# Kernel tuning notes

Measured on AMD Instinct MI355X. Metric: run time of the kernel, lower is better.

## Reference

```python
import jax, jax.numpy as jnp
import numpy as np

EPS = 1e-5
QMAX = 127.0

def activation_quant(x):
    # per-token (last-dim) abs-max int8 fake-quant
    x_max = jnp.clip(jnp.max(jnp.abs(x), axis=-1, keepdims=True), EPS, None)
    scale = QMAX / x_max
    q = jnp.clip(jnp.round(x * scale), -128.0, 127.0)
    return q / scale

def setup_inputs() -> dict:
    key = jax.random.key(0)
    kx, kw = jax.random.split(key)
    x = jax.random.normal(kx, (4, 8192, 2048), dtype=jnp.float32)
    # ternary {-1, 0, 1} weight, stored int8 in torch, cast to float for the GEMM
    W = jax.random.randint(kw, (2048, 2048), -1, 2).astype(jnp.float32)  # [out, in]
    return {"x": x, "W": W}

def reference(x, W):
    # straight-through estimator form: x + sg(quant(x) - x)
    x_quant = x + jax.lax.stop_gradient(activation_quant(x) - x)
    # y = x_quant @ W.T  (F.linear)
    return jnp.einsum('bsd,od->bso', x_quant, W)
```

## Files before the change

### kernel.cpp

```cpp
#include <hip/hip_runtime.h>

typedef int v4i __attribute__((ext_vector_type(4)));

#define KDIM 2048
#define NDIM 2048

#define GLOAD16(g, l) __builtin_amdgcn_global_load_lds(                      \
    (const __attribute__((address_space(1))) void*)(g),                      \
    (__attribute__((address_space(3))) void*)(l), 16, 0, 0)


__device__ __forceinline__ int pack4q(float4 v, float s) {
  int a = __float2int_rn(v.x * s);
  int b = __float2int_rn(v.y * s);
  int c = __float2int_rn(v.z * s);
  int d = __float2int_rn(v.w * s);
  a = max(-128, min(127, a)); b = max(-128, min(127, b));
  c = max(-128, min(127, c)); d = max(-128, min(127, d));
  return (a & 0xff) | ((b & 0xff) << 8) | ((c & 0xff) << 16) | ((d & 0xff) << 24);
}

__global__ __launch_bounds__(256) void quant_rows(const float* __restrict__ x,
                                                  signed char* __restrict__ q,
                                                  float* __restrict__ rscale) {
  const int row = blockIdx.x;
  const float4* xr = (const float4*)(x + (size_t)row * KDIM);
  float4 v0 = xr[threadIdx.x];
  float4 v1 = xr[256 + threadIdx.x];
  float m = fmaxf(fmaxf(fabsf(v0.x), fabsf(v0.y)), fmaxf(fabsf(v0.z), fabsf(v0.w)));
  m = fmaxf(m, fmaxf(fmaxf(fabsf(v1.x), fabsf(v1.y)), fmaxf(fabsf(v1.z), fabsf(v1.w))));
  #pragma unroll
  for (int off = 32; off > 0; off >>= 1) m = fmaxf(m, __shfl_xor(m, off));
  __shared__ float red[4];
  if ((threadIdx.x & 63) == 0) red[threadIdx.x >> 6] = m;
  __syncthreads();
  float xmax = fmaxf(fmaxf(red[0], red[1]), fmaxf(red[2], red[3]));
  xmax = fmaxf(xmax, 1e-5f);
  const float scale = 127.0f / xmax;
  int* qr = (int*)(q + (size_t)row * KDIM);
  qr[threadIdx.x] = pack4q(v0, scale);
  qr[256 + threadIdx.x] = pack4q(v1, scale);
  if (threadIdx.x == 0) rscale[row] = xmax * (1.0f / 127.0f);
}

__global__ __launch_bounds__(256) void quant_w(const float* __restrict__ W,
                                               signed char* __restrict__ Wq) {
  const int i = blockIdx.x * 256 + threadIdx.x;
  float4 v = ((const float4*)W)[i];
  int a = (int)v.x, b = (int)v.y, c = (int)v.z, d = (int)v.w;
  ((int*)Wq)[i] = (a & 0xff) | ((b & 0xff) << 8) | ((c & 0xff) << 16) | ((d & 0xff) << 24);
}


#define VM4 asm volatile("s_waitcnt vmcnt(4)" ::: "memory")
#define VM0 asm volatile("s_waitcnt vmcnt(0)" ::: "memory")
#define VMNONE

#define STAGE_AB(U, T)                                                       \
  GLOAD16(sa + (T) * 64, lds + (U) * 32768 + dstw);                          \
  GLOAD16(sa + (T) * 64 + 128 * KDIM, lds + (U) * 32768 + 8192 + dstw);      \
  GLOAD16(sb + (T) * 64, lds + (U) * 32768 + 16384 + dstw);                  \
  GLOAD16(sb + (T) * 64 + 128 * KDIM, lds + (U) * 32768 + 24576 + dstw);

#define DECLSET(P) v4i P##b0, P##b1, P##b2, P##b3,                           \
                       P##a0, P##a1, P##a2, P##a3, P##a4, P##a5, P##a6, P##a7;

#define READSET(U, P)                                                        \
  P##b0 = *(const v4i*)(lds + (U) * 32768 + bRd);                            \
  P##b1 = *(const v4i*)(lds + (U) * 32768 + bRd + 1024);                     \
  P##b2 = *(const v4i*)(lds + (U) * 32768 + bRd + 2048);                     \
  P##b3 = *(const v4i*)(lds + (U) * 32768 + bRd + 3072);                     \
  P##a0 = *(const v4i*)(lds + (U) * 32768 + aRd);                            \
  P##a1 = *(const v4i*)(lds + (U) * 32768 + aRd + 1024);                     \
  P##a2 = *(const v4i*)(lds + (U) * 32768 + aRd + 2048);                     \
  P##a3 = *(const v4i*)(lds + (U) * 32768 + aRd + 3072);                     \
  P##a4 = *(const v4i*)(lds + (U) * 32768 + aRd + 4096);                     \
  P##a5 = *(const v4i*)(lds + (U) * 32768 + aRd + 5120);                     \
  P##a6 = *(const v4i*)(lds + (U) * 32768 + aRd + 6144);                     \
  P##a7 = *(const v4i*)(lds + (U) * 32768 + aRd + 7168);

#define MF1(m, n, A, BF) acc[m][n] = __builtin_amdgcn_mfma_i32_16x16x64_i8((A), (BF), acc[m][n], 0, 0, 0);
#define MFROW(m, A, P)                                                       \
  MF1(m, 0, A, P##b0) MF1(m, 1, A, P##b1) MF1(m, 2, A, P##b2) MF1(m, 3, A, P##b3)
#define MFSET(P)                                                             \
  __builtin_amdgcn_s_setprio(1);                                             \
  MFROW(0, P##a0, P) MFROW(1, P##a1, P) MFROW(2, P##a2, P)                   \
  MFROW(3, P##a3, P) MFROW(4, P##a4, P) MFROW(5, P##a5, P)                   \
  MFROW(6, P##a6, P) MFROW(7, P##a7, P)                                      \
  __builtin_amdgcn_s_setprio(0);

#define KTILE(U, T, CUR, NXT, DOREAD, DOSTAGE, VMEND)                        \
  {                                                                          \
    if (DOREAD) { READSET((((U) + 1) & 3), NXT) }                            \
    if (DOSTAGE) { STAGE_AB((((U) + 3) & 3), (T) + 3) }                      \
    __builtin_amdgcn_sched_barrier(0);    \
    MFSET(CUR)                                                               \
    __builtin_amdgcn_sched_barrier(0);                                       \
    VMEND;                                                                   \
    __builtin_amdgcn_s_barrier();                                            \
    __builtin_amdgcn_sched_barrier(0);           \
  }

__global__ __launch_bounds__(512, 2) void gemm_i8(const signed char* __restrict__ A,
                                                  const signed char* __restrict__ B,
                                                  const float* __restrict__ rscale,
                                                  float* __restrict__ C) {
  __shared__ __align__(16) signed char lds[131072];
  const int bid = blockIdx.x;
  const int lid = (bid & 7) * 128 + (bid >> 3);
  const int bm = lid >> 3;
  const int bn = lid & 7;
  const int tid = threadIdx.x;
  const int wid = tid >> 6;
  const int lane = tid & 63;
  const int wr = wid >> 2, wc = wid & 3;

  const int srow = wid * 16 + (lane >> 2);
  const int scol = (((lane & 3) ^ ((lane >> 3) & 3)) << 4);
  const signed char* sa = A + (size_t)(bm * 256 + srow) * KDIM + scol;
  const signed char* sb = B + (size_t)(bn * 256 + srow) * KDIM + scol;
  const int dstw = wid << 10;

  const int rslot = (((lane >> 4) ^ ((lane >> 1) & 3)) << 4);
  const int aRd = (wr * 128 + (lane & 15)) * 64 + rslot;
  const int bRd = 16384 + (wc * 64 + (lane & 15)) * 64 + rslot;

  v4i acc[8][4] = {};
  DECLSET(fX) DECLSET(fY)

  STAGE_AB(0, 0)
  STAGE_AB(1, 1)
  STAGE_AB(2, 2)
  VM4;
  __builtin_amdgcn_s_barrier();
  __builtin_amdgcn_sched_barrier(0);
  READSET(0, fX)

  for (int ti = 0; ti < 7; ++ti) {
    const int t = ti * 4;
    KTILE(0, t + 0, fX, fY, 1, 1, VM4)
    KTILE(1, t + 1, fY, fX, 1, 1, VM4)
    KTILE(2, t + 2, fX, fY, 1, 1, VM4)
    KTILE(3, t + 3, fY, fX, 1, 1, VM4)
  }
  KTILE(0, 28, fX, fY, 1, 1, VM4)
  KTILE(1, 29, fY, fX, 1, 0, VM0)
  KTILE(2, 30, fX, fY, 1, 0, VMNONE)
  KTILE(3, 31, fY, fX, 0, 0, VMNONE)

  const int col0 = bn * 256 + wc * 64 + (lane & 15);
  const int rbase = bm * 256 + wr * 128 + ((lane >> 4) << 2);
  #pragma unroll
  for (int m = 0; m < 8; ++m) {
    #pragma unroll
    for (int r = 0; r < 4; ++r) {
      const int row = rbase + m * 16 + r;
      const float s = rscale[row];
      float* crow = C + (size_t)row * NDIM + col0;
      #pragma unroll
      for (int n = 0; n < 4; ++n) crow[n * 16] = (float)acc[m][n][r] * s;
    }
  }
}

extern "C" void kernel_launch(void* const* d_in, const int* in_sizes, int n_in,
                              void* d_out, int out_size, void* d_ws, size_t ws_size,
                              hipStream_t stream) {
  const float* x = (const float*)d_in[0];
  const float* W = (const float*)d_in[1];
  float* out = (float*)d_out;
  const int M = in_sizes[0] / KDIM;

  signed char* q = (signed char*)d_ws;
  signed char* Wq = q + (size_t)M * KDIM;
  float* rscale = (float*)(Wq + (size_t)NDIM * KDIM);

  quant_rows<<<M, 256, 0, stream>>>(x, q, rscale);
  quant_w<<<(NDIM * KDIM / 4) / 256, 256, 0, stream>>>(W, Wq);
  gemm_i8<<<(M / 256) * (NDIM / 256), 512, 0, stream>>>(q, Wq, rscale, out);
}
```

Baseline: 240.4 us.

## Prepack weights into MFMA fragment layout and load B directly to registers

The weight-quant kernel now writes W in a fragment-ordered layout, so each lane's 16-byte B operand is contiguous. The GEMM loads B straight from global memory into registers instead of staging it through LDS. A is staged alone in a 3-deep LDS ring of 16 KB buffers, which shrinks shared memory from 128 KB to 48 KB and removes B's LDS traffic. The cost is that B fragments are fetched from global/L2 by every wave that needs them, with only one tile of register prefetch to hide that latency.

```diff
diff --git a/kernel.cpp b/kernel.cpp
--- a/kernel.cpp
+++ b/kernel.cpp
@@ -43,69 +43,83 @@
   if (threadIdx.x == 0) rscale[row] = xmax * (1.0f / 127.0f);
 }
 
-__global__ __launch_bounds__(256) void quant_w(const float* __restrict__ W,
-                                               signed char* __restrict__ Wq) {
-  const int i = blockIdx.x * 256 + threadIdx.x;
-  float4 v = ((const float4*)W)[i];
-  int a = (int)v.x, b = (int)v.y, c = (int)v.z, d = (int)v.w;
-  ((int*)Wq)[i] = (a & 0xff) | ((b & 0xff) << 8) | ((c & 0xff) << 16) | ((d & 0xff) << 24);
+__global__ __launch_bounds__(256) void quant_w_pack(const float* __restrict__ W,
+                                                    signed char* __restrict__ Bp) {
+  const int gid = blockIdx.x * 256 + threadIdx.x;
+  const int lane = gid & 63;
+  const int f = gid >> 6;
+  const int nf = f & 15;
+  const int bkt = f >> 4;
+  const int kt = bkt & 31;
+  const int bn = bkt >> 5;
+  const int row = bn * 256 + nf * 16 + (lane & 15);
+  const int k0 = kt * 64 + (lane >> 4) * 16;
+  const float* src = W + (size_t)row * KDIM + k0;
+  int out[4];
+  #pragma unroll
+  for (int j = 0; j < 4; ++j) {
+    int b0 = (int)src[j * 4 + 0] & 0xff;
+    int b1 = (int)src[j * 4 + 1] & 0xff;
+    int b2 = (int)src[j * 4 + 2] & 0xff;
+    int b3 = (int)src[j * 4 + 3] & 0xff;
+    out[j] = b0 | (b1 << 8) | (b2 << 16) | (b3 << 24);
+  }
+  v4i o = { out[0], out[1], out[2], out[3] };
+  *(v4i*)(Bp + (size_t)gid * 16) = o;
 }
 
 
-#define VM4 asm volatile("s_waitcnt vmcnt(4)" ::: "memory")
+#define VM2 asm volatile("s_waitcnt vmcnt(2)" ::: "memory")
 #define VM0 asm volatile("s_waitcnt vmcnt(0)" ::: "memory")
 #define VMNONE
 
-#define STAGE_AB(U, T)                                                       \
-  GLOAD16(sa + (T) * 64, lds + (U) * 32768 + dstw);                          \
-  GLOAD16(sa + (T) * 64 + 128 * KDIM, lds + (U) * 32768 + 8192 + dstw);      \
-  GLOAD16(sb + (T) * 64, lds + (U) * 32768 + 16384 + dstw);                  \
-  GLOAD16(sb + (T) * 64 + 128 * KDIM, lds + (U) * 32768 + 24576 + dstw);
+#define STAGE(U, T)                                                          \
+  GLOAD16(sa + (T) * 64,             lds + (U) * 16384 + dstw);              \
+  GLOAD16(sa + (T) * 64 + 16 * KDIM, lds + (U) * 16384 + 1024 + dstw);
 
-#define DECLSET(P) v4i P##b0, P##b1, P##b2, P##b3,                           \
-                       P##a0, P##a1, P##a2, P##a3, P##a4, P##a5, P##a6, P##a7;
-
-#define READSET(U, P)                                                        \
-  P##b0 = *(const v4i*)(lds + (U) * 32768 + bRd);                            \
-  P##b1 = *(const v4i*)(lds + (U) * 32768 + bRd + 1024);                     \
-  P##b2 = *(const v4i*)(lds + (U) * 32768 + bRd + 2048);                     \
-  P##b3 = *(const v4i*)(lds + (U) * 32768 + bRd + 3072);                     \
-  P##a0 = *(const v4i*)(lds + (U) * 32768 + aRd);                            \
-  P##a1 = *(const v4i*)(lds + (U) * 32768 + aRd + 1024);                     \
-  P##a2 = *(const v4i*)(lds + (U) * 32768 + aRd + 2048);                     \
-  P##a3 = *(const v4i*)(lds + (U) * 32768 + aRd + 3072);                     \
-  P##a4 = *(const v4i*)(lds + (U) * 32768 + aRd + 4096);                     \
-  P##a5 = *(const v4i*)(lds + (U) * 32768 + aRd + 5120);                     \
-  P##a6 = *(const v4i*)(lds + (U) * 32768 + aRd + 6144);                     \
-  P##a7 = *(const v4i*)(lds + (U) * 32768 + aRd + 7168);
+#define LOADB(P, T)                                                          \
+  P##0 = *(const v4i*)(bp + (size_t)(T) * 16384);                            \
+  P##1 = *(const v4i*)(bp + (size_t)(T) * 16384 + 1024);                     \
+  P##2 = *(const v4i*)(bp + (size_t)(T) * 16384 + 2048);                     \
+  P##3 = *(const v4i*)(bp + (size_t)(T) * 16384 + 3072);
 
 #define MF1(m, n, A, BF) acc[m][n] = __builtin_amdgcn_mfma_i32_16x16x64_i8((A), (BF), acc[m][n], 0, 0, 0);
-#define MFROW(m, A, P)                                                       \
-  MF1(m, 0, A, P##b0) MF1(m, 1, A, P##b1) MF1(m, 2, A, P##b2) MF1(m, 3, A, P##b3)
-#define MFSET(P)                                                             \
+
+#define MFSET(CB)                                                            \
   __builtin_amdgcn_s_setprio(1);                                             \
-  MFROW(0, P##a0, P) MFROW(1, P##a1, P) MFROW(2, P##a2, P)                   \
-  MFROW(3, P##a3, P) MFROW(4, P##a4, P) MFROW(5, P##a5, P)                   \
-  MFROW(6, P##a6, P) MFROW(7, P##a7, P)                                      \
+  MF1(0, 0, a0, CB##0) MF1(0, 1, a0, CB##1) MF1(0, 2, a0, CB##2) MF1(0, 3, a0, CB##3) \
+  MF1(1, 0, a1, CB##0) MF1(1, 1, a1, CB##1) MF1(1, 2, a1, CB##2) MF1(1, 3, a1, CB##3) \
+  MF1(2, 0, a2, CB##0) MF1(2, 1, a2, CB##1) MF1(2, 2, a2, CB##2) MF1(2, 3, a2, CB##3) \
+  MF1(3, 0, a3, CB##0) MF1(3, 1, a3, CB##1) MF1(3, 2, a3, CB##2) MF1(3, 3, a3, CB##3) \
+  MF1(4, 0, a4, CB##0) MF1(4, 1, a4, CB##1) MF1(4, 2, a4, CB##2) MF1(4, 3, a4, CB##3) \
+  MF1(5, 0, a5, CB##0) MF1(5, 1, a5, CB##1) MF1(5, 2, a5, CB##2) MF1(5, 3, a5, CB##3) \
+  MF1(6, 0, a6, CB##0) MF1(6, 1, a6, CB##1) MF1(6, 2, a6, CB##2) MF1(6, 3, a6, CB##3) \
+  MF1(7, 0, a7, CB##0) MF1(7, 1, a7, CB##1) MF1(7, 2, a7, CB##2) MF1(7, 3, a7, CB##3) \
   __builtin_amdgcn_s_setprio(0);
 
-#define KTILE(U, T, CUR, NXT, DOREAD, DOSTAGE, VMEND)                        \
+#define KTILE(U, T, CB, NB, DOB, DOSTAGE, VMEND)                             \
   {                                                                          \
-    if (DOREAD) { READSET((((U) + 1) & 3), NXT) }                            \
-    if (DOSTAGE) { STAGE_AB((((U) + 3) & 3), (T) + 3) }                      \
-    __builtin_amdgcn_sched_barrier(0);    \
-    MFSET(CUR)                                                               \
-    __builtin_amdgcn_sched_barrier(0);                                       \
+    if (DOB) { LOADB(NB, (T) + 1) }                                          \
+    if (DOSTAGE) { STAGE((((U) + 2) % 3), (T) + 2) }                         \
+    v4i a0 = *(const v4i*)(lds + (U) * 16384 + aRd);                         \
+    v4i a1 = *(const v4i*)(lds + (U) * 16384 + aRd + 1024);                  \
+    v4i a2 = *(const v4i*)(lds + (U) * 16384 + aRd + 2048);                  \
+    v4i a3 = *(const v4i*)(lds + (U) * 16384 + aRd + 3072);                  \
+    v4i a4 = *(const v4i*)(lds + (U) * 16384 + aRd + 4096);                  \
+    v4i a5 = *(const v4i*)(lds + (U) * 16384 + aRd + 5120);                  \
+    v4i a6 = *(const v4i*)(lds + (U) * 16384 + aRd + 6144);                  \
+    v4i a7 = *(const v4i*)(lds + (U) * 16384 + aRd + 7168);                  \
+    MFSET(CB)                                                                \
     VMEND;                                                                   \
     __builtin_amdgcn_s_barrier();                                            \
-    __builtin_amdgcn_sched_barrier(0);           \
+    __builtin_amdgcn_sched_barrier(0);                                       \
   }
 
 __global__ __launch_bounds__(512, 2) void gemm_i8(const signed char* __restrict__ A,
-                                                  const signed char* __restrict__ B,
+                                                  const signed char* __restrict__ Bp,
                                                   const float* __restrict__ rscale,
                                                   float* __restrict__ C) {
-  __shared__ __align__(16) signed char lds[131072];
+  __shared__ __align__(16) signed char lds[3 * 16384];
   const int bid = blockIdx.x;
   const int lid = (bid & 7) * 128 + (bid >> 3);
   const int bm = lid >> 3;
@@ -115,38 +129,36 @@
   const int lane = tid & 63;
   const int wr = wid >> 2, wc = wid & 3;
 
-  const int srow = wid * 16 + (lane >> 2);
   const int scol = (((lane & 3) ^ ((lane >> 3) & 3)) << 4);
-  const signed char* sa = A + (size_t)(bm * 256 + srow) * KDIM + scol;
-  const signed char* sb = B + (size_t)(bn * 256 + srow) * KDIM + scol;
-  const int dstw = wid << 10;
+  const signed char* sa = A + (size_t)(bm * 256 + wid * 32 + (lane >> 2)) * KDIM + scol;
+  const int dstw = wid << 11;
 
   const int rslot = (((lane >> 4) ^ ((lane >> 1) & 3)) << 4);
   const int aRd = (wr * 128 + (lane & 15)) * 64 + rslot;
-  const int bRd = 16384 + (wc * 64 + (lane & 15)) * 64 + rslot;
+
+  const signed char* bp = Bp + ((size_t)(bn * 32) * 16 + wc * 4) * 1024 + lane * 16;
 
   v4i acc[8][4] = {};
-  DECLSET(fX) DECLSET(fY)
+  v4i fX0, fX1, fX2, fX3, fY0, fY1, fY2, fY3;
 
-  STAGE_AB(0, 0)
-  STAGE_AB(1, 1)
-  STAGE_AB(2, 2)
-  VM4;
+  STAGE(0, 0)
+  LOADB(fX, 0)
+  STAGE(1, 1)
+  VM2;
   __builtin_amdgcn_s_barrier();
   __builtin_amdgcn_sched_barrier(0);
-  READSET(0, fX)
 
-  for (int ti = 0; ti < 7; ++ti) {
-    const int t = ti * 4;
-    KTILE(0, t + 0, fX, fY, 1, 1, VM4)
-    KTILE(1, t + 1, fY, fX, 1, 1, VM4)
-    KTILE(2, t + 2, fX, fY, 1, 1, VM4)
-    KTILE(3, t + 3, fY, fX, 1, 1, VM4)
+  for (int ti = 0; ti < 5; ++ti) {
+    const int t = ti * 6;
+    KTILE(0, t + 0, fX, fY, 1, 1, VM2)
+    KTILE(1, t + 1, fY, fX, 1, 1, VM2)
+    KTILE(2, t + 2, fX, fY, 1, 1, VM2)
+    KTILE(0, t + 3, fY, fX, 1, 1, VM2)
+    KTILE(1, t + 4, fX, fY, 1, 1, VM2)
+    KTILE(2, t + 5, fY, fX, 1, 1, VM2)
   }
-  KTILE(0, 28, fX, fY, 1, 1, VM4)
-  KTILE(1, 29, fY, fX, 1, 0, VM0)
-  KTILE(2, 30, fX, fY, 1, 0, VMNONE)
-  KTILE(3, 31, fY, fX, 0, 0, VMNONE)
+  KTILE(0, 30, fX, fY, 1, 0, VM0)
+  KTILE(1, 31, fY, fX, 0, 0, VMNONE)
 
   const int col0 = bn * 256 + wc * 64 + (lane & 15);
   const int rbase = bm * 256 + wr * 128 + ((lane >> 4) << 2);
@@ -172,10 +184,10 @@
   const int M = in_sizes[0] / KDIM;
 
   signed char* q = (signed char*)d_ws;
-  signed char* Wq = q + (size_t)M * KDIM;
-  float* rscale = (float*)(Wq + (size_t)NDIM * KDIM);
+  signed char* Bp = q + (size_t)M * KDIM;
+  float* rscale = (float*)(Bp + (size_t)NDIM * KDIM);
 
   quant_rows<<<M, 256, 0, stream>>>(x, q, rscale);
-  quant_w<<<(NDIM * KDIM / 4) / 256, 256, 0, stream>>>(W, Wq);
-  gemm_i8<<<(M / 256) * (NDIM / 256), 512, 0, stream>>>(q, Wq, rscale, out);
+  quant_w_pack<<<(NDIM * KDIM / 16) / 256, 256, 0, stream>>>(W, Bp);
+  gemm_i8<<<(M / 256) * (NDIM / 256), 512, 0, stream>>>(q, Bp, rscale, out);
 }
```

Result: slower. 280.4 us (+16.6%).
